# Kernel optimization log

Measured on AMD Instinct MI355X. Metric: run time of the kernel, lower is better.

Reference implementation:

```python
import jax, jax.numpy as jnp
import numpy as np

N = 6144
HIDDEN = 48
HEADS = 3
HEAD = HIDDEN // HEADS


def setup_inputs() -> dict:
    key = jax.random.key(0)
    ks = jax.random.split(key, 8)
    s = 1.0 / np.sqrt(HIDDEN)
    A = (jax.random.uniform(ks[0], (N, N)) < 0.05).astype(jnp.float32)
    h = jax.random.normal(ks[1], (N, HIDDEN), dtype=jnp.float32)
    Wq = jax.random.normal(ks[2], (HIDDEN, HIDDEN), dtype=jnp.float32) * s
    Wk = jax.random.normal(ks[3], (HIDDEN, HIDDEN), dtype=jnp.float32) * s
    Wv = jax.random.normal(ks[4], (HIDDEN, HIDDEN), dtype=jnp.float32) * s
    bq = jnp.zeros((HIDDEN,), jnp.float32)
    bk = jnp.zeros((HIDDEN,), jnp.float32)
    bv = jnp.zeros((HIDDEN,), jnp.float32)
    return {"A": A, "h": h, "Wq": Wq, "bq": bq, "Wk": Wk, "bk": bk, "Wv": Wv, "bv": bv}


def reference(A, h, Wq, bq, Wk, bk, Wv, bv):
    n = h.shape[0]
    # QKV projections (torch Linear: x @ W.T + b)
    q = (h @ Wq.T + bq).reshape(n, HEADS, HEAD).transpose(1, 0, 2)  # [H,N,d]
    k = (h @ Wk.T + bk).reshape(n, HEADS, HEAD).transpose(1, 0, 2)
    v = (h @ Wv.T + bv).reshape(n, HEADS, HEAD).transpose(1, 0, 2)
    # scores = (q k^T) * A / N**(-0.5)  == (q k^T) * A * sqrt(N)  (faithful to source)
    scale = jnp.asarray(n, h.dtype) ** 0.5
    scores = jnp.einsum("hnd,hmd->hnm", q, k) * A[None, :, :] * scale
    scores = jax.nn.softmax(scores, axis=2)
    out = jnp.einsum("hnm,hmd->hnd", scores, v)  # [H,N,d]
    out = out.transpose(1, 0, 2).reshape(n, HIDDEN)
    return (out, scores)
```

## Files before the change

kernel.cpp:

```cpp
#include <hip/hip_runtime.h>
#include <math.h>

#define NN   6144
#define HID  48
#define BLK  512
#define RPB  4
#define CAP  448
#define CTOT (RPB*CAP)
#define NSL  42
#define SCALE 78.38367176906175f

typedef float vf4 __attribute__((ext_vector_type(4)));

__global__ __launch_bounds__(256)
void qkv_kernel(const float* __restrict__ h,
                const float* __restrict__ Wq, const float* __restrict__ bq,
                const float* __restrict__ Wk, const float* __restrict__ bk,
                const float* __restrict__ Wv, const float* __restrict__ bv,
                float* __restrict__ qw, float* __restrict__ kw, float* __restrict__ vw) {
    int idx = blockIdx.x * blockDim.x + threadIdx.x;
    int i = idx / HID, c = idx % HID;
    const float4* h4  = (const float4*)(h + (size_t)i * HID);
    const float4* wq4 = (const float4*)(Wq + (size_t)c * HID);
    const float4* wk4 = (const float4*)(Wk + (size_t)c * HID);
    const float4* wv4 = (const float4*)(Wv + (size_t)c * HID);
    float aq = 0.f, ak = 0.f, av = 0.f;
    #pragma unroll
    for (int r = 0; r < HID / 4; ++r) {
        float4 hv = h4[r];
        float4 q4 = wq4[r], k4 = wk4[r], v4 = wv4[r];
        aq = fmaf(hv.x, q4.x, aq); aq = fmaf(hv.y, q4.y, aq);
        aq = fmaf(hv.z, q4.z, aq); aq = fmaf(hv.w, q4.w, aq);
        ak = fmaf(hv.x, k4.x, ak); ak = fmaf(hv.y, k4.y, ak);
        ak = fmaf(hv.z, k4.z, ak); ak = fmaf(hv.w, k4.w, ak);
        av = fmaf(hv.x, v4.x, av); av = fmaf(hv.y, v4.y, av);
        av = fmaf(hv.z, v4.z, av); av = fmaf(hv.w, v4.w, av);
    }
    aq += bq[c]; ak += bk[c]; av += bv[c];
    int head = c >> 4, d = c & 15;
    size_t off = ((size_t)head * NN + i) * 16 + d;
    qw[off] = aq; kw[off] = ak; vw[off] = av;
}

__global__ __launch_bounds__(256)
void vtot_kernel(const float* __restrict__ vw, float* __restrict__ vtot) {
    int c = blockIdx.x;
    int head = c >> 4, d = c & 15;
    float s = 0.f;
    for (int j = threadIdx.x; j < NN; j += 256)
        s += vw[((size_t)head * NN + j) * 16 + d];
    #pragma unroll
    for (int o = 32; o; o >>= 1) s += __shfl_xor(s, o, 64);
    __shared__ float red[4];
    int wid = threadIdx.x >> 6, lane = threadIdx.x & 63;
    if (lane == 0) red[wid] = s;
    __syncthreads();
    if (threadIdx.x == 0) vtot[c] = red[0] + red[1] + red[2] + red[3];
}

__device__ __forceinline__ float maxw(const float* w, int idx) {
    float m = 0.f;
    #pragma unroll
    for (int k = 0; k < 8; ++k) m = fmaxf(m, w[k * 12 + idx]);
    return m;
}
__device__ __forceinline__ float sumw(const float* w, int idx) {
    float s = 0.f;
    #pragma unroll
    for (int k = 0; k < 8; ++k) s += w[k * 12 + idx];
    return s;
}

__global__ __launch_bounds__(BLK)
void attn_kernel(const float* __restrict__ A,
                 const float* __restrict__ qw, const float* __restrict__ kw,
                 const float* __restrict__ vw, const float* __restrict__ vtot,
                 float* __restrict__ out) {
    __shared__ int   list[CTOT];
    __shared__ float sc[3][CTOT];
    __shared__ __align__(16) float qs[RPB * 48];
    __shared__ float accL[RPB * 52];
    __shared__ float wredM[8 * 12];
    __shared__ float wredL[8 * 12];
    __shared__ unsigned wlo[8], whi[8];

    const int i0 = blockIdx.x * RPB;
    const int tid = threadIdx.x;
    const int wid = tid >> 6, lane = tid & 63;

    if (tid < RPB * 48) {
        int r = tid / 48, c = tid % 48;
        int hh = c >> 4, d = c & 15;
        qs[tid] = qw[((size_t)hh * NN + (i0 + r)) * 16 + d];
    }
    if (tid < RPB * 52) accL[tid] = 0.f;

    unsigned long long amask = 0ull;
    #pragma unroll
    for (int r = 0; r < RPB; ++r) {
        const vf4* Ar = (const vf4*)(A + (size_t)(i0 + r) * NN);
        #pragma unroll
        for (int c = 0; c < 3; ++c) {
            vf4 a4 = __builtin_nontemporal_load(&Ar[tid + c * BLK]);
            int p = r * 16 + c * 4;
            if (a4.x != 0.f) amask |= 1ull << (p + 0);
            if (a4.y != 0.f) amask |= 1ull << (p + 1);
            if (a4.z != 0.f) amask |= 1ull << (p + 2);
            if (a4.w != 0.f) amask |= 1ull << (p + 3);
        }
    }
    unsigned m0 = (unsigned)(amask & 0xFFFull);
    unsigned m1 = (unsigned)((amask >> 16) & 0xFFFull);
    unsigned m2 = (unsigned)((amask >> 32) & 0xFFFull);
    unsigned m3 = (unsigned)((amask >> 48) & 0xFFFull);
    unsigned lo = (unsigned)__popc(m0) | ((unsigned)__popc(m1) << 16);
    unsigned hi = (unsigned)__popc(m2) | ((unsigned)__popc(m3) << 16);

    unsigned ilo = lo, ihi = hi;
    #pragma unroll
    for (int o = 1; o < 64; o <<= 1) {
        unsigned plo = __shfl_up(ilo, o, 64);
        unsigned phi = __shfl_up(ihi, o, 64);
        if (lane >= o) { ilo += plo; ihi += phi; }
    }
    if (lane == 63) { wlo[wid] = ilo; whi[wid] = ihi; }
    __syncthreads();
    unsigned blo = ilo - lo, bhi = ihi - hi;
    unsigned tlo = 0, thi = 0;
    #pragma unroll
    for (int w = 0; w < 8; ++w) {
        unsigned a = wlo[w], b = whi[w];
        if (w < wid) { blo += a; bhi += b; }
        tlo += a; thi += b;
    }
    const int C0 = min((int)(tlo & 0xFFFFu), CAP), C1 = min((int)(tlo >> 16), CAP);
    const int C2 = min((int)(thi & 0xFFFFu), CAP), C3 = min((int)(thi >> 16), CAP);
    const int cum1 = C0, cum2 = C0 + C1, cum3 = cum2 + C2;
    int bs[4] = {(int)(blo & 0xFFFFu), (int)(blo >> 16),
                 (int)(bhi & 0xFFFFu), (int)(bhi >> 16)};
    int cu[5] = {0, cum1, cum2, cum3, cum3 + C3};
    unsigned mr[4] = {m0, m1, m2, m3};
    int Cr4[4] = {C0, C1, C2, C3};

    #pragma unroll
    for (int r = 0; r < RPB; ++r) {
        unsigned m = mr[r];
        int b = bs[r];
        while (m) {
            int p = __ffs(m) - 1; m &= m - 1;
            if (b < CAP) list[cu[r] + b] = 4 * (tid + (p >> 2) * BLK) + (p & 3);
            ++b;
        }
    }
    __syncthreads();

    {
        const int q4 = tid >> 2, part = tid & 3;
        #pragma unroll
        for (int r = 0; r < RPB; ++r) {
            float4 qv0 = ((const float4*)(qs + r * 48 +  0))[part];
            float4 qv1 = ((const float4*)(qs + r * 48 + 16))[part];
            float4 qv2 = ((const float4*)(qs + r * 48 + 32))[part];
            float mx0 = 0.f, mx1 = 0.f, mx2 = 0.f;
            for (int e = cu[r] + q4; e < cu[r + 1]; e += (BLK >> 2)) {
                int j = list[e];
                float4 k0 = ((const float4*)(kw + ((size_t)0 * NN + j) * 16))[part];
                float4 k1 = ((const float4*)(kw + ((size_t)1 * NN + j) * 16))[part];
                float4 k2 = ((const float4*)(kw + ((size_t)2 * NN + j) * 16))[part];
                float d0 = k0.x * qv0.x; d0 = fmaf(k0.y, qv0.y, d0);
                d0 = fmaf(k0.z, qv0.z, d0); d0 = fmaf(k0.w, qv0.w, d0);
                float d1 = k1.x * qv1.x; d1 = fmaf(k1.y, qv1.y, d1);
                d1 = fmaf(k1.z, qv1.z, d1); d1 = fmaf(k1.w, qv1.w, d1);
                float d2 = k2.x * qv2.x; d2 = fmaf(k2.y, qv2.y, d2);
                d2 = fmaf(k2.z, qv2.z, d2); d2 = fmaf(k2.w, qv2.w, d2);
                d0 += __shfl_xor(d0, 1, 64); d0 += __shfl_xor(d0, 2, 64);
                d1 += __shfl_xor(d1, 1, 64); d1 += __shfl_xor(d1, 2, 64);
                d2 += __shfl_xor(d2, 1, 64); d2 += __shfl_xor(d2, 2, 64);
                float s0 = d0 * SCALE, s1 = d1 * SCALE, s2 = d2 * SCALE;
                if (part == 0) sc[0][e] = s0;
                else if (part == 1) sc[1][e] = s1;
                else if (part == 2) sc[2][e] = s2;
                mx0 = fmaxf(mx0, s0);
                mx1 = fmaxf(mx1, s1);
                mx2 = fmaxf(mx2, s2);
            }
            #pragma unroll
            for (int o = 32; o; o >>= 1) {
                mx0 = fmaxf(mx0, __shfl_xor(mx0, o, 64));
                mx1 = fmaxf(mx1, __shfl_xor(mx1, o, 64));
                mx2 = fmaxf(mx2, __shfl_xor(mx2, o, 64));
            }
            if (lane == 0) {
                wredM[wid * 12 + r * 3 + 0] = mx0;
                wredM[wid * 12 + r * 3 + 1] = mx1;
                wredM[wid * 12 + r * 3 + 2] = mx2;
            }
        }
    }
    __syncthreads();

    #pragma unroll
    for (int r = 0; r < RPB; ++r) {
        float M0 = maxw(wredM, r * 3 + 0);
        float M1 = maxw(wredM, r * 3 + 1);
        float M2 = maxw(wredM, r * 3 + 2);
        float l0 = 0.f, l1 = 0.f, l2 = 0.f;
        for (int e = cu[r] + tid; e < cu[r + 1]; e += BLK) {
            float p0 = __expf(sc[0][e] - M0); sc[0][e] = p0; l0 += p0;
            float p1 = __expf(sc[1][e] - M1); sc[1][e] = p1; l1 += p1;
            float p2 = __expf(sc[2][e] - M2); sc[2][e] = p2; l2 += p2;
        }
        #pragma unroll
        for (int o = 32; o; o >>= 1) {
            l0 += __shfl_xor(l0, o, 64);
            l1 += __shfl_xor(l1, o, 64);
            l2 += __shfl_xor(l2, o, 64);
        }
        if (lane == 0) {
            wredL[wid * 12 + r * 3 + 0] = l0;
            wredL[wid * 12 + r * 3 + 1] = l1;
            wredL[wid * 12 + r * 3 + 2] = l2;
        }
    }
    __syncthreads();

    float* Pp = out + (size_t)NN * HID;

    #pragma unroll
    for (int r = 0; r < RPB; ++r) {
        float M0 = maxw(wredM, r * 3 + 0), M1 = maxw(wredM, r * 3 + 1), M2 = maxw(wredM, r * 3 + 2);
        float z0 = __expf(-M0), z1 = __expf(-M1), z2 = __expf(-M2);
        float fc = (float)(NN - Cr4[r]);
        float iv0 = 1.0f / (sumw(wredL, r * 3 + 0) + fc * z0);
        float iv1 = 1.0f / (sumw(wredL, r * 3 + 1) + fc * z1);
        float iv2 = 1.0f / (sumw(wredL, r * 3 + 2) + fc * z2);
        float zi0 = z0 * iv0, zi1 = z1 * iv1, zi2 = z2 * iv2;
        int b = bs[r];
        unsigned m = mr[r];
        size_t rowoff = (size_t)(i0 + r) * NN;
        #pragma unroll
        for (int c = 0; c < 3; ++c) {
            vf4 P0, P1, P2;
            #pragma unroll
            for (int e = 0; e < 4; ++e) {
                int p = c * 4 + e;
                bool nz = (m >> p) & 1u;
                if (nz && b < CAP) {
                    int slot = cu[r] + b;
                    P0[e] = sc[0][slot] * iv0;
                    P1[e] = sc[1][slot] * iv1;
                    P2[e] = sc[2][slot] * iv2;
                } else {
                    P0[e] = zi0; P1[e] = zi1; P2[e] = zi2;
                }
                b += nz ? 1 : 0;
            }
            __builtin_nontemporal_store(P0, &((vf4*)(Pp + 0 * (size_t)NN * NN + rowoff))[tid + c * BLK]);
            __builtin_nontemporal_store(P1, &((vf4*)(Pp + 1 * (size_t)NN * NN + rowoff))[tid + c * BLK]);
            __builtin_nontemporal_store(P2, &((vf4*)(Pp + 2 * (size_t)NN * NN + rowoff))[tid + c * BLK]);
        }
    }

    if (tid < NSL * 12) {
        int s = tid % 12, a = tid / 12;
        int hh = s >> 2, rr4 = s & 3;
        const float* vbase = vw + (size_t)hh * NN * 16 + rr4 * 4;
        #pragma unroll
        for (int r = 0; r < RPB; ++r) {
            float zz = __expf(-maxw(wredM, r * 3 + hh));
            float ax = 0.f, ay = 0.f, az = 0.f, aw = 0.f;
            #pragma unroll 2
            for (int e = cu[r] + a; e < cu[r + 1]; e += NSL) {
                int j = list[e];
                float w = sc[hh][e] - zz;
                float4 vv = *(const float4*)(vbase + (size_t)j * 16);
                ax = fmaf(w, vv.x, ax);
                ay = fmaf(w, vv.y, ay);
                az = fmaf(w, vv.z, az);
                aw = fmaf(w, vv.w, aw);
            }
            int cb = r * 52 + hh * 16 + rr4 * 4;
            atomicAdd(&accL[cb + 0], ax);
            atomicAdd(&accL[cb + 1], ay);
            atomicAdd(&accL[cb + 2], az);
            atomicAdd(&accL[cb + 3], aw);
        }
    }
    __syncthreads();

    if (tid < RPB * 48) {
        int r = tid / 48, c = tid % 48, hh = c >> 4;
        float M = maxw(wredM, r * 3 + hh);
        float z = __expf(-M);
        float iv = 1.0f / (sumw(wredL, r * 3 + hh) + (float)(NN - Cr4[r]) * z);
        out[(size_t)(i0 + r) * HID + c] = (accL[r * 52 + c] + z * vtot[c]) * iv;
    }
}

extern "C" void kernel_launch(void* const* d_in, const int* in_sizes, int n_in,
                              void* d_out, int out_size, void* d_ws, size_t ws_size,
                              hipStream_t stream) {
    const float* A  = (const float*)d_in[0];
    const float* h  = (const float*)d_in[1];
    const float* Wq = (const float*)d_in[2];
    const float* bq = (const float*)d_in[3];
    const float* Wk = (const float*)d_in[4];
    const float* bk = (const float*)d_in[5];
    const float* Wv = (const float*)d_in[6];
    const float* bv = (const float*)d_in[7];
    float* out = (float*)d_out;
    float* ws  = (float*)d_ws;

    float* qw   = ws;
    float* kw   = ws + (size_t)3 * NN * 16;
    float* vw   = ws + (size_t)6 * NN * 16;
    float* vtot = ws + (size_t)9 * NN * 16;

    qkv_kernel<<<(NN * HID) / 256, 256, 0, stream>>>(h, Wq, bq, Wk, bk, Wv, bv, qw, kw, vw);
    vtot_kernel<<<HID, 256, 0, stream>>>(vw, vtot);
    attn_kernel<<<NN / RPB, BLK, 0, stream>>>(A, qw, kw, vw, vtot, out);
}
```

Measured before the change: 631.6 us.

## Fuse softmax exp/sum pass into PV gather, recompute exp in P store

Removes the separate pass that exponentiated the scores in LDS and reduced row sums across warps. The exp and its row sum are now computed inside the sparse PV gather loop, with the sums gathered through LDS atomics. The dense probability store recomputes exp from the raw scores, and the PV output is written before the large P store. This drops one barrier and one LDS read/write pass, at the cost of doing exp twice per nonzero and of atomic contention on the sum buffer. A reordering of two FMAs in the QKV kernel is also included, which slightly changes rounding.

```diff
diff --git a/kernel.cpp b/kernel.cpp
--- a/kernel.cpp
+++ b/kernel.cpp
@@ -34,7 +34,7 @@
         ak = fmaf(hv.x, k4.x, ak); ak = fmaf(hv.y, k4.y, ak);
         ak = fmaf(hv.z, k4.z, ak); ak = fmaf(hv.w, k4.w, ak);
         av = fmaf(hv.x, v4.x, av); av = fmaf(hv.y, v4.y, av);
-        av = fmaf(hv.z, v4.z, av); av = fmaf(hv.w, v4.w, av);
+        av = fmaf(hv.w, v4.w, av); av = fmaf(hv.z, v4.z, av);
     }
     aq += bq[c]; ak += bk[c]; av += bv[c];
     int head = c >> 4, d = c & 15;
@@ -63,12 +63,6 @@
     #pragma unroll
     for (int k = 0; k < 8; ++k) m = fmaxf(m, w[k * 12 + idx]);
     return m;
-}
-__device__ __forceinline__ float sumw(const float* w, int idx) {
-    float s = 0.f;
-    #pragma unroll
-    for (int k = 0; k < 8; ++k) s += w[k * 12 + idx];
-    return s;
 }
 
 __global__ __launch_bounds__(BLK)
@@ -80,8 +74,8 @@
     __shared__ float sc[3][CTOT];
     __shared__ __align__(16) float qs[RPB * 48];
     __shared__ float accL[RPB * 52];
+    __shared__ float lAcc[12];
     __shared__ float wredM[8 * 12];
-    __shared__ float wredL[8 * 12];
     __shared__ unsigned wlo[8], whi[8];
 
     const int i0 = blockIdx.x * RPB;
@@ -94,6 +88,7 @@
         qs[tid] = qw[((size_t)hh * NN + (i0 + r)) * 16 + d];
     }
     if (tid < RPB * 52) accL[tid] = 0.f;
+    if (tid < 12) lAcc[tid] = 0.f;
 
     unsigned long long amask = 0ull;
     #pragma unroll
@@ -199,30 +194,45 @@
     }
     __syncthreads();
 
-    #pragma unroll
-    for (int r = 0; r < RPB; ++r) {
-        float M0 = maxw(wredM, r * 3 + 0);
-        float M1 = maxw(wredM, r * 3 + 1);
-        float M2 = maxw(wredM, r * 3 + 2);
-        float l0 = 0.f, l1 = 0.f, l2 = 0.f;
-        for (int e = cu[r] + tid; e < cu[r + 1]; e += BLK) {
-            float p0 = __expf(sc[0][e] - M0); sc[0][e] = p0; l0 += p0;
-            float p1 = __expf(sc[1][e] - M1); sc[1][e] = p1; l1 += p1;
-            float p2 = __expf(sc[2][e] - M2); sc[2][e] = p2; l2 += p2;
-        }
-        #pragma unroll
-        for (int o = 32; o; o >>= 1) {
-            l0 += __shfl_xor(l0, o, 64);
-            l1 += __shfl_xor(l1, o, 64);
-            l2 += __shfl_xor(l2, o, 64);
-        }
-        if (lane == 0) {
-            wredL[wid * 12 + r * 3 + 0] = l0;
-            wredL[wid * 12 + r * 3 + 1] = l1;
-            wredL[wid * 12 + r * 3 + 2] = l2;
-        }
-    }
-    __syncthreads();
+    if (tid < NSL * 12) {
+        int s = tid % 12, a = tid / 12;
+        int hh = s >> 2, rr4 = s & 3;
+        const float* vbase = vw + (size_t)hh * NN * 16 + rr4 * 4;
+        #pragma unroll
+        for (int r = 0; r < RPB; ++r) {
+            float M = maxw(wredM, r * 3 + hh);
+            float zz = __expf(-M);
+            float ax = 0.f, ay = 0.f, az = 0.f, aw = 0.f;
+            float lp = 0.f;
+            #pragma unroll 2
+            for (int e = cu[r] + a; e < cu[r + 1]; e += NSL) {
+                int j = list[e];
+                float p = __expf(sc[hh][e] - M);
+                float w = p - zz;
+                lp += p;
+                float4 vv = *(const float4*)(vbase + (size_t)j * 16);
+                ax = fmaf(w, vv.x, ax);
+                ay = fmaf(w, vv.y, ay);
+                az = fmaf(w, vv.z, az);
+                aw = fmaf(w, vv.w, aw);
+            }
+            int cb = r * 52 + hh * 16 + rr4 * 4;
+            atomicAdd(&accL[cb + 0], ax);
+            atomicAdd(&accL[cb + 1], ay);
+            atomicAdd(&accL[cb + 2], az);
+            atomicAdd(&accL[cb + 3], aw);
+            if (rr4 == 0) atomicAdd(&lAcc[r * 3 + hh], lp);
+        }
+    }
+    __syncthreads();
+
+    if (tid < RPB * 48) {
+        int r = tid / 48, c = tid % 48, hh = c >> 4;
+        float M = maxw(wredM, r * 3 + hh);
+        float z = __expf(-M);
+        float iv = 1.0f / (lAcc[r * 3 + hh] + (float)(NN - Cr4[r]) * z);
+        out[(size_t)(i0 + r) * HID + c] = (accL[r * 52 + c] + z * vtot[c]) * iv;
+    }
 
     float* Pp = out + (size_t)NN * HID;
 
@@ -231,9 +241,9 @@
         float M0 = maxw(wredM, r * 3 + 0), M1 = maxw(wredM, r * 3 + 1), M2 = maxw(wredM, r * 3 + 2);
         float z0 = __expf(-M0), z1 = __expf(-M1), z2 = __expf(-M2);
         float fc = (float)(NN - Cr4[r]);
-        float iv0 = 1.0f / (sumw(wredL, r * 3 + 0) + fc * z0);
-        float iv1 = 1.0f / (sumw(wredL, r * 3 + 1) + fc * z1);
-        float iv2 = 1.0f / (sumw(wredL, r * 3 + 2) + fc * z2);
+        float iv0 = 1.0f / (lAcc[r * 3 + 0] + fc * z0);
+        float iv1 = 1.0f / (lAcc[r * 3 + 1] + fc * z1);
+        float iv2 = 1.0f / (lAcc[r * 3 + 2] + fc * z2);
         float zi0 = z0 * iv0, zi1 = z1 * iv1, zi2 = z2 * iv2;
         int b = bs[r];
         unsigned m = mr[r];
@@ -247,9 +257,9 @@
                 bool nz = (m >> p) & 1u;
                 if (nz && b < CAP) {
                     int slot = cu[r] + b;
-                    P0[e] = sc[0][slot] * iv0;
-                    P1[e] = sc[1][slot] * iv1;
-                    P2[e] = sc[2][slot] * iv2;
+                    P0[e] = __expf(sc[0][slot] - M0) * iv0;
+                    P1[e] = __expf(sc[1][slot] - M1) * iv1;
+                    P2[e] = __expf(sc[2][slot] - M2) * iv2;
                 } else {
                     P0[e] = zi0; P1[e] = zi1; P2[e] = zi2;
                 }
@@ -259,41 +269,6 @@
             __builtin_nontemporal_store(P1, &((vf4*)(Pp + 1 * (size_t)NN * NN + rowoff))[tid + c * BLK]);
             __builtin_nontemporal_store(P2, &((vf4*)(Pp + 2 * (size_t)NN * NN + rowoff))[tid + c * BLK]);
         }
-    }
-
-    if (tid < NSL * 12) {
-        int s = tid % 12, a = tid / 12;
-        int hh = s >> 2, rr4 = s & 3;
-        const float* vbase = vw + (size_t)hh * NN * 16 + rr4 * 4;
-        #pragma unroll
-        for (int r = 0; r < RPB; ++r) {
-            float zz = __expf(-maxw(wredM, r * 3 + hh));
-            float ax = 0.f, ay = 0.f, az = 0.f, aw = 0.f;
-            #pragma unroll 2
-            for (int e = cu[r] + a; e < cu[r + 1]; e += NSL) {
-                int j = list[e];
-                float w = sc[hh][e] - zz;
-                float4 vv = *(const float4*)(vbase + (size_t)j * 16);
-                ax = fmaf(w, vv.x, ax);
-                ay = fmaf(w, vv.y, ay);
-                az = fmaf(w, vv.z, az);
-                aw = fmaf(w, vv.w, aw);
-            }
-            int cb = r * 52 + hh * 16 + rr4 * 4;
-            atomicAdd(&accL[cb + 0], ax);
-            atomicAdd(&accL[cb + 1], ay);
-            atomicAdd(&accL[cb + 2], az);
-            atomicAdd(&accL[cb + 3], aw);
-        }
-    }
-    __syncthreads();
-
-    if (tid < RPB * 48) {
-        int r = tid / 48, c = tid % 48, hh = c >> 4;
-        float M = maxw(wredM, r * 3 + hh);
-        float z = __expf(-M);
-        float iv = 1.0f / (sumw(wredL, r * 3 + hh) + (float)(NN - Cr4[r]) * z);
-        out[(size_t)(i0 + r) * HID + c] = (accL[r * 52 + c] + z * vtot[c]) * iv;
     }
 }
 
```

Result: no change. 628.8 us (-0.4%).
